# Performance work log

Measured on AMD Instinct MI355X. Metric: run time of the kernel, lower is better.

## Reference

```python
import jax, jax.numpy as jnp
import numpy as np

B, H, N, D = 4, 16, 2048, 128  # batch, num_head, maxlen, head_dim (qkdim == vdim)
EPS = 1e-6


def _act(x):
    # '1+elu' kernel feature map
    return jax.nn.elu(x) + 1.0


def _simple_rms_norm(x):
    # SimpleRMSNorm over the last dim: x / sqrt(mean(x^2) + eps), no learned scale
    ms = jnp.mean(jnp.square(x), axis=-1, keepdims=True)
    return x * jax.lax.rsqrt(ms + EPS)


def setup_inputs() -> dict:
    key = jax.random.key(0)
    kq, kk, kv, km = jax.random.split(key, 4)
    Q = jax.random.normal(kq, (B, H, N, D), dtype=jnp.float32)
    K = jax.random.normal(kk, (B, H, N, D), dtype=jnp.float32)
    V = jax.random.normal(kv, (B, H, N, D), dtype=jnp.float32)
    mask = jax.random.uniform(km, (B, N), dtype=jnp.float32)
    return {"Q": Q, "K": K, "V": V, "mask": mask}


def reference(Q, K, V, mask):
    m = mask[:, None, :, None]           # (B, 1, N, 1)
    Qf = _act(Q)                          # (B, H, N, D)
    Kf = _act(K) * m                      # masked feature-mapped keys
    Vf = V * m                            # masked values
    # non-causal linear attention: KV = sum_n K_n (x) V_n ; out = Q @ KV
    KV = jnp.einsum('bhnd,bhne->bhde', Kf, Vf)    # (B, H, D, D)
    out = jnp.einsum('bhde,bhnd->bhne', KV, Qf)   # (B, H, N, D)
    return _simple_rms_norm(out)
```

## Files before the change

### kernel.cpp

```cpp
#include <hip/hip_runtime.h>
#include <hip/hip_bf16.h>

#define NBH 64
#define NSEQ 2048
#define DD 128
#define EPS 1e-6f

typedef __bf16 bf16x8 __attribute__((ext_vector_type(8)));
typedef __bf16 bf16x4 __attribute__((ext_vector_type(4)));
typedef float  f32x4  __attribute__((ext_vector_type(4)));

__device__ __forceinline__ float elu1(float x) {
    return x > 0.f ? x + 1.f : __expf(x);
}

__device__ __forceinline__ int swz(int r) {
    return ((r >> 2) & 7) ^ ((r & 1) << 2);
}

__global__ __launch_bounds__(512, 4) void kv_partial_kernel(
    const float* __restrict__ K, const float* __restrict__ V,
    const float* __restrict__ mask, float* __restrict__ part)
{
    __shared__ __bf16 KfT[2][128 * 64];
    __shared__ __bf16 VfT[2][128 * 64];
    __shared__ float  mloc[256];

    const int s    = blockIdx.x;
    const int bh   = blockIdx.y;
    const int b    = bh >> 4;
    const int t    = threadIdx.x;
    const int lane = t & 63;
    const int w    = t >> 6;
    const int quad = lane >> 4;
    const int col  = lane & 15;
    const int n0   = s * 256;

    const int isV = t >> 8;
    const int c   = t & 31;
    const int rg  = (t >> 5) & 7;

    const f32x4* S4 = (const f32x4*)((isV ? V : K) + ((size_t)bh * NSEQ + n0) * DD);
    __bf16* myT = isV ? &VfT[0][0] : &KfT[0][0];

    f32x4 acc[8];
    #pragma unroll
    for (int nt = 0; nt < 8; ++nt) acc[nt] = (f32x4){0.f, 0.f, 0.f, 0.f};

    const int arow = w * 16 + col;
    const int aidx = arow * 64 + (swz(arow) << 3);
    int bidx[8];
    #pragma unroll
    for (int nt = 0; nt < 8; ++nt) {
        int r = nt * 16 + col;
        bidx[nt] = r * 64 + (swz(r) << 3);
    }

    f32x4 xr[8];

    auto load_tile = [&](int tile) {
        #pragma unroll
        for (int j = 0; j < 8; ++j)
            xr[j] = S4[(tile * 64 + rg * 8 + j) * 32 + c];
    };

    auto stage = [&](int buf, int tile) {
        float ml[8];
        #pragma unroll
        for (int j = 0; j < 8; ++j) ml[j] = mloc[tile * 64 + rg * 8 + j];
        __bf16* dst = myT + buf * (128 * 64);
        #pragma unroll
        for (int i = 0; i < 4; ++i) {
            bf16x8 xc;
            if (!isV) {
                #pragma unroll
                for (int j = 0; j < 8; ++j) xc[j] = (__bf16)(elu1(xr[j][i]) * ml[j]);
            } else {
                #pragma unroll
                for (int j = 0; j < 8; ++j) xc[j] = (__bf16)(xr[j][i] * ml[j]);
            }
            int d = 4 * c + i;
            *(bf16x8*)&dst[d * 64 + ((rg ^ swz(d)) << 3)] = xc;
        }
    };

    auto mfma_tile = [&](int buf) {
        const __bf16* Vb = &VfT[buf][0];
        const __bf16* Kb = &KfT[buf][0];
        #pragma unroll
        for (int kk = 0; kk < 2; ++kk) {
            int k0 = kk * 32 + quad * 8;
            bf16x8 a = *(bf16x8*)&Vb[aidx ^ k0];
            #pragma unroll
            for (int nt = 0; nt < 8; ++nt) {
                bf16x8 bb = *(bf16x8*)&Kb[bidx[nt] ^ k0];
                acc[nt] = __builtin_amdgcn_mfma_f32_16x16x32_bf16(a, bb, acc[nt], 0, 0, 0);
            }
        }
    };

    float mf = 0.f;
    if (t < 256) mf = mask[b * NSEQ + n0 + t];
    load_tile(0);
    if (t < 256) mloc[t] = mf;
    __syncthreads();
    stage(0, 0);
    __syncthreads();

    #pragma unroll
    for (int tile = 0; tile < 4; ++tile) {
        if (tile < 3) load_tile(tile + 1);
        mfma_tile(tile & 1);
        if (tile < 3) {
            stage((tile + 1) & 1, tile + 1);
            __syncthreads();
        }
    }

    float* po = part + (((size_t)bh * 8 + s) << 14);
    #pragma unroll
    for (int r = 0; r < 4; ++r) {
        int e = w * 16 + quad * 4 + r;
        #pragma unroll
        for (int nt = 0; nt < 8; ++nt)
            po[e * 128 + nt * 16 + col] = acc[nt][r];
    }
}

__global__ __launch_bounds__(256) void kv_reduce_kernel(
    const float* __restrict__ part, __bf16* __restrict__ kvt)
{
    int gid = blockIdx.x * 256 + threadIdx.x;
    int i   = gid * 4;
    int bh  = i >> 14;
    int ii  = i & 16383;
    const float* p = part + (((size_t)bh * 8) << 14) + ii;
    f32x4 sum = (f32x4){0.f, 0.f, 0.f, 0.f};
    #pragma unroll
    for (int s = 0; s < 8; ++s)
        sum += *(const f32x4*)(p + ((size_t)s << 14));
    bf16x4 o;
    o[0] = (__bf16)sum[0]; o[1] = (__bf16)sum[1];
    o[2] = (__bf16)sum[2]; o[3] = (__bf16)sum[3];
    *(bf16x4*)&kvt[i] = o;
}

__global__ __launch_bounds__(256, 4) void qkv_norm_kernel(
    const float* __restrict__ Q, const __bf16* __restrict__ kvt,
    float* __restrict__ out)
{
    __shared__ __bf16 KVT[128 * 136];

    const int bh   = blockIdx.y;
    const int row0 = blockIdx.x * 64;
    const int t    = threadIdx.x;
    const int lane = t & 63;
    const int w    = t >> 6;
    const int quad = lane >> 4;
    const int col  = lane & 15;

    const int row = row0 + w * 16 + col;
    const f32x4* q4 = (const f32x4*)(Q + ((size_t)bh * NSEQ + row) * DD);
    f32x4 qr[8];
    #pragma unroll
    for (int kk = 0; kk < 4; ++kk) {
        qr[2 * kk]     = q4[kk * 8 + quad * 2];
        qr[2 * kk + 1] = q4[kk * 8 + quad * 2 + 1];
    }

    {
        const __bf16* src = kvt + ((size_t)bh << 14);
        #pragma unroll
        for (int i = 0; i < 8; ++i) {
            int idx = i * 256 + t;
            int e   = idx >> 4;
            int dd  = (idx & 15) * 8;
            *(bf16x8*)&KVT[e * 136 + dd] = *(const bf16x8*)&src[e * 128 + dd];
        }
    }
    __syncthreads();

    bf16x8 a[4];
    #pragma unroll
    for (int kk = 0; kk < 4; ++kk) {
        #pragma unroll
        for (int h = 0; h < 2; ++h) {
            f32x4 q = qr[2 * kk + h];
            #pragma unroll
            for (int u = 0; u < 4; ++u)
                a[kk][h * 4 + u] = (__bf16)elu1(q[u]);
        }
    }

    f32x4 acc[8];
    #pragma unroll
    for (int et = 0; et < 8; ++et) acc[et] = (f32x4){0.f, 0.f, 0.f, 0.f};

    #pragma unroll
    for (int kk = 0; kk < 4; ++kk) {
        int k0 = kk * 32 + quad * 8;
        #pragma unroll
        for (int et = 0; et < 8; ++et) {
            bf16x8 bb = *(bf16x8*)&KVT[(et * 16 + col) * 136 + k0];
            acc[et] = __builtin_amdgcn_mfma_f32_16x16x32_bf16(a[kk], bb, acc[et], 0, 0, 0);
        }
    }

    float* ob = out + ((size_t)bh * NSEQ + row0) * DD;
    #pragma unroll
    for (int r = 0; r < 4; ++r) {
        float p = 0.f;
        #pragma unroll
        for (int et = 0; et < 8; ++et) p += acc[et][r] * acc[et][r];
        p += __shfl_xor(p, 1);
        p += __shfl_xor(p, 2);
        p += __shfl_xor(p, 4);
        p += __shfl_xor(p, 8);
        float scale = rsqrtf(p * (1.0f / 128.0f) + EPS);
        int orow = w * 16 + quad * 4 + r;
        #pragma unroll
        for (int et = 0; et < 8; ++et)
            ob[orow * DD + et * 16 + col] = acc[et][r] * scale;
    }
}

extern "C" void kernel_launch(void* const* d_in, const int* in_sizes, int n_in,
                              void* d_out, int out_size, void* d_ws, size_t ws_size,
                              hipStream_t stream) {
    const float* Q    = (const float*)d_in[0];
    const float* K    = (const float*)d_in[1];
    const float* V    = (const float*)d_in[2];
    const float* mask = (const float*)d_in[3];
    float* out = (float*)d_out;

    float*  part = (float*)d_ws;
    __bf16* kvt  = (__bf16*)((char*)d_ws + (size_t)NBH * 8 * 16384 * 4);

    kv_partial_kernel<<<dim3(8, NBH), 512, 0, stream>>>(K, V, mask, part);
    kv_reduce_kernel<<<1024, 256, 0, stream>>>(part, kvt);
    qkv_norm_kernel<<<dim3(32, NBH), 256, 0, stream>>>(Q, kvt, out);
}
```

Measured before the change: 236.6 us.

## Single-buffer KV partial LDS with 2D warp tiling; process two row chunks per Q block

The KV partial kernel drops double buffering in favor of a single LDS buffer guarded by extra barriers. Halving LDS use lets launch bounds ask for more resident blocks. Its warp tiling changes from 16-row strips to a 64x32 2D tile, so each warp loads fewer LDS fragments per MFMA. The Q/KV kernel now handles 128 rows per block in two chunks, reusing the staged KV^T tile and prefetching the second chunk's Q, at the cost of half as many blocks and more registers.

```diff
diff --git a/kernel.cpp b/kernel.cpp
--- a/kernel.cpp
+++ b/kernel.cpp
@@ -14,16 +14,17 @@
     return x > 0.f ? x + 1.f : __expf(x);
 }
 
-__device__ __forceinline__ int swz(int r) {
-    return ((r >> 2) & 7) ^ ((r & 1) << 2);
-}
-
-__global__ __launch_bounds__(512, 4) void kv_partial_kernel(
+__device__ __forceinline__ int ldsidx64(int r, int k0) {
+    int sw = ((((r >> 2) & 7) ^ ((r & 1) << 2)) << 3);
+    return r * 64 + (sw ^ k0);
+}
+
+__global__ __launch_bounds__(512, 6) void kv_partial_kernel(
     const float* __restrict__ K, const float* __restrict__ V,
     const float* __restrict__ mask, float* __restrict__ part)
 {
-    __shared__ __bf16 KfT[2][128 * 64];
-    __shared__ __bf16 VfT[2][128 * 64];
+    __shared__ __bf16 KfT[128 * 64];
+    __shared__ __bf16 VfT[128 * 64];
     __shared__ float  mloc[256];
 
     const int s    = blockIdx.x;
@@ -35,26 +36,19 @@
     const int quad = lane >> 4;
     const int col  = lane & 15;
     const int n0   = s * 256;
+    const int we   = w >> 2;
+    const int wd   = w & 3;
 
     const int isV = t >> 8;
     const int c   = t & 31;
     const int rg  = (t >> 5) & 7;
 
     const f32x4* S4 = (const f32x4*)((isV ? V : K) + ((size_t)bh * NSEQ + n0) * DD);
-    __bf16* myT = isV ? &VfT[0][0] : &KfT[0][0];
+    __bf16* myT = isV ? VfT : KfT;
 
     f32x4 acc[8];
     #pragma unroll
-    for (int nt = 0; nt < 8; ++nt) acc[nt] = (f32x4){0.f, 0.f, 0.f, 0.f};
-
-    const int arow = w * 16 + col;
-    const int aidx = arow * 64 + (swz(arow) << 3);
-    int bidx[8];
-    #pragma unroll
-    for (int nt = 0; nt < 8; ++nt) {
-        int r = nt * 16 + col;
-        bidx[nt] = r * 64 + (swz(r) << 3);
-    }
+    for (int i = 0; i < 8; ++i) acc[i] = (f32x4){0.f, 0.f, 0.f, 0.f};
 
     f32x4 xr[8];
 
@@ -64,11 +58,10 @@
             xr[j] = S4[(tile * 64 + rg * 8 + j) * 32 + c];
     };
 
-    auto stage = [&](int buf, int tile) {
+    auto stage = [&](int tile) {
         float ml[8];
         #pragma unroll
         for (int j = 0; j < 8; ++j) ml[j] = mloc[tile * 64 + rg * 8 + j];
-        __bf16* dst = myT + buf * (128 * 64);
         #pragma unroll
         for (int i = 0; i < 4; ++i) {
             bf16x8 xc;
@@ -80,50 +73,45 @@
                 for (int j = 0; j < 8; ++j) xc[j] = (__bf16)(xr[j][i] * ml[j]);
             }
             int d = 4 * c + i;
-            *(bf16x8*)&dst[d * 64 + ((rg ^ swz(d)) << 3)] = xc;
+            *(bf16x8*)&myT[ldsidx64(d, rg << 3)] = xc;
         }
     };
 
-    auto mfma_tile = [&](int buf) {
-        const __bf16* Vb = &VfT[buf][0];
-        const __bf16* Kb = &KfT[buf][0];
+    auto mfma_tile = [&]() {
         #pragma unroll
         for (int kk = 0; kk < 2; ++kk) {
             int k0 = kk * 32 + quad * 8;
-            bf16x8 a = *(bf16x8*)&Vb[aidx ^ k0];
-            #pragma unroll
-            for (int nt = 0; nt < 8; ++nt) {
-                bf16x8 bb = *(bf16x8*)&Kb[bidx[nt] ^ k0];
-                acc[nt] = __builtin_amdgcn_mfma_f32_16x16x32_bf16(a, bb, acc[nt], 0, 0, 0);
+            bf16x8 b0 = *(bf16x8*)&KfT[ldsidx64(wd * 32 + col, k0)];
+            bf16x8 b1 = *(bf16x8*)&KfT[ldsidx64(wd * 32 + 16 + col, k0)];
+            #pragma unroll
+            for (int at = 0; at < 4; ++at) {
+                bf16x8 aa = *(bf16x8*)&VfT[ldsidx64(we * 64 + at * 16 + col, k0)];
+                acc[at * 2]     = __builtin_amdgcn_mfma_f32_16x16x32_bf16(aa, b0, acc[at * 2], 0, 0, 0);
+                acc[at * 2 + 1] = __builtin_amdgcn_mfma_f32_16x16x32_bf16(aa, b1, acc[at * 2 + 1], 0, 0, 0);
             }
         }
     };
 
-    float mf = 0.f;
-    if (t < 256) mf = mask[b * NSEQ + n0 + t];
+    if (t < 256) mloc[t] = mask[b * NSEQ + n0 + t];
     load_tile(0);
-    if (t < 256) mloc[t] = mf;
     __syncthreads();
-    stage(0, 0);
+    stage(0);
     __syncthreads();
 
-    #pragma unroll
-    for (int tile = 0; tile < 4; ++tile) {
-        if (tile < 3) load_tile(tile + 1);
-        mfma_tile(tile & 1);
-        if (tile < 3) {
-            stage((tile + 1) & 1, tile + 1);
-            __syncthreads();
-        }
-    }
+    load_tile(1); mfma_tile(); __syncthreads(); stage(1); __syncthreads();
+    load_tile(2); mfma_tile(); __syncthreads(); stage(2); __syncthreads();
+    load_tile(3); mfma_tile(); __syncthreads(); stage(3); __syncthreads();
+    mfma_tile();
 
     float* po = part + (((size_t)bh * 8 + s) << 14);
     #pragma unroll
-    for (int r = 0; r < 4; ++r) {
-        int e = w * 16 + quad * 4 + r;
-        #pragma unroll
-        for (int nt = 0; nt < 8; ++nt)
-            po[e * 128 + nt * 16 + col] = acc[nt][r];
+    for (int at = 0; at < 4; ++at) {
+        #pragma unroll
+        for (int r = 0; r < 4; ++r) {
+            int e = we * 64 + at * 16 + quad * 4 + r;
+            po[e * 128 + wd * 32 + col]      = acc[at * 2][r];
+            po[e * 128 + wd * 32 + 16 + col] = acc[at * 2 + 1][r];
+        }
     }
 }
 
@@ -152,20 +140,21 @@
     __shared__ __bf16 KVT[128 * 136];
 
     const int bh   = blockIdx.y;
-    const int row0 = blockIdx.x * 64;
+    const int row0 = blockIdx.x * 128;
     const int t    = threadIdx.x;
     const int lane = t & 63;
     const int w    = t >> 6;
     const int quad = lane >> 4;
     const int col  = lane & 15;
 
-    const int row = row0 + w * 16 + col;
-    const f32x4* q4 = (const f32x4*)(Q + ((size_t)bh * NSEQ + row) * DD);
-    f32x4 qr[8];
+    const int qrow = w * 16 + col;
+    const f32x4* q4 = (const f32x4*)(Q + ((size_t)bh * NSEQ + row0 + qrow) * DD);
+
+    f32x4 qr0[8];
     #pragma unroll
     for (int kk = 0; kk < 4; ++kk) {
-        qr[2 * kk]     = q4[kk * 8 + quad * 2];
-        qr[2 * kk + 1] = q4[kk * 8 + quad * 2 + 1];
+        qr0[2 * kk]     = q4[kk * 8 + quad * 2];
+        qr0[2 * kk + 1] = q4[kk * 8 + quad * 2 + 1];
     }
 
     {
@@ -185,42 +174,66 @@
     for (int kk = 0; kk < 4; ++kk) {
         #pragma unroll
         for (int h = 0; h < 2; ++h) {
-            f32x4 q = qr[2 * kk + h];
+            f32x4 q = qr0[2 * kk + h];
             #pragma unroll
             for (int u = 0; u < 4; ++u)
                 a[kk][h * 4 + u] = (__bf16)elu1(q[u]);
         }
     }
 
-    f32x4 acc[8];
-    #pragma unroll
-    for (int et = 0; et < 8; ++et) acc[et] = (f32x4){0.f, 0.f, 0.f, 0.f};
-
+    f32x4 qr1[8];
     #pragma unroll
     for (int kk = 0; kk < 4; ++kk) {
-        int k0 = kk * 32 + quad * 8;
-        #pragma unroll
-        for (int et = 0; et < 8; ++et) {
-            bf16x8 bb = *(bf16x8*)&KVT[(et * 16 + col) * 136 + k0];
-            acc[et] = __builtin_amdgcn_mfma_f32_16x16x32_bf16(a[kk], bb, acc[et], 0, 0, 0);
-        }
+        qr1[2 * kk]     = q4[2048 + kk * 8 + quad * 2];
+        qr1[2 * kk + 1] = q4[2048 + kk * 8 + quad * 2 + 1];
     }
 
     float* ob = out + ((size_t)bh * NSEQ + row0) * DD;
-    #pragma unroll
-    for (int r = 0; r < 4; ++r) {
-        float p = 0.f;
-        #pragma unroll
-        for (int et = 0; et < 8; ++et) p += acc[et][r] * acc[et][r];
-        p += __shfl_xor(p, 1);
-        p += __shfl_xor(p, 2);
-        p += __shfl_xor(p, 4);
-        p += __shfl_xor(p, 8);
-        float scale = rsqrtf(p * (1.0f / 128.0f) + EPS);
-        int orow = w * 16 + quad * 4 + r;
-        #pragma unroll
-        for (int et = 0; et < 8; ++et)
-            ob[orow * DD + et * 16 + col] = acc[et][r] * scale;
+
+    #pragma unroll
+    for (int chunk = 0; chunk < 2; ++chunk) {
+        f32x4 acc[8];
+        #pragma unroll
+        for (int et = 0; et < 8; ++et) acc[et] = (f32x4){0.f, 0.f, 0.f, 0.f};
+
+        #pragma unroll
+        for (int kk = 0; kk < 4; ++kk) {
+            int k0 = kk * 32 + quad * 8;
+            #pragma unroll
+            for (int et = 0; et < 8; ++et) {
+                bf16x8 bb = *(bf16x8*)&KVT[(et * 16 + col) * 136 + k0];
+                acc[et] = __builtin_amdgcn_mfma_f32_16x16x32_bf16(a[kk], bb, acc[et], 0, 0, 0);
+            }
+        }
+
+        #pragma unroll
+        for (int r = 0; r < 4; ++r) {
+            float p = 0.f;
+            #pragma unroll
+            for (int et = 0; et < 8; ++et) p += acc[et][r] * acc[et][r];
+            p += __shfl_xor(p, 1);
+            p += __shfl_xor(p, 2);
+            p += __shfl_xor(p, 4);
+            p += __shfl_xor(p, 8);
+            float scale = rsqrtf(p * (1.0f / 128.0f) + EPS);
+            int orow = chunk * 64 + w * 16 + quad * 4 + r;
+            #pragma unroll
+            for (int et = 0; et < 8; ++et)
+                ob[orow * DD + et * 16 + col] = acc[et][r] * scale;
+        }
+
+        if (chunk == 0) {
+            #pragma unroll
+            for (int kk = 0; kk < 4; ++kk) {
+                #pragma unroll
+                for (int h = 0; h < 2; ++h) {
+                    f32x4 q = qr1[2 * kk + h];
+                    #pragma unroll
+                    for (int u = 0; u < 4; ++u)
+                        a[kk][h * 4 + u] = (__bf16)elu1(q[u]);
+                }
+            }
+        }
     }
 }
 
@@ -238,5 +251,5 @@
 
     kv_partial_kernel<<<dim3(8, NBH), 512, 0, stream>>>(K, V, mask, part);
     kv_reduce_kernel<<<1024, 256, 0, stream>>>(part, kvt);
-    qkv_norm_kernel<<<dim3(32, NBH), 256, 0, stream>>>(Q, kvt, out);
-}
+    qkv_norm_kernel<<<dim3(16, NBH), 256, 0, stream>>>(Q, kvt, out);
+}
```

Measured after the change: 251.5 us. 6.3% more time.

## Fuse three kernels into one cooperative kernel with grid-wide syncs

Applied to the files above, without the earlier changes.

Replaces the partial-KV, reduce, and Q·KV+RMSNorm launches with a single cooperative kernel of 512 blocks that uses grid.sync() between the phases. Each block then handles 256 query rows in two chunks, and shared memory is unioned across the phases. This removes two kernel launch gaps and the tail idle time between them. In exchange it pays for two grid-wide barriers and lower parallelism in the final phase (512 blocks instead of 2048), and it falls back to the three-kernel path if the cooperative launch fails.

```diff
diff --git a/kernel.cpp b/kernel.cpp
--- a/kernel.cpp
+++ b/kernel.cpp
@@ -1,5 +1,8 @@
 #include <hip/hip_runtime.h>
 #include <hip/hip_bf16.h>
+#include <hip/hip_cooperative_groups.h>
+
+namespace cg = cooperative_groups;
 
 #define NBH 64
 #define NSEQ 2048
@@ -18,13 +21,24 @@
     return ((r >> 2) & 7) ^ ((r & 1) << 2);
 }
 
-__global__ __launch_bounds__(512, 4) void kv_partial_kernel(
-    const float* __restrict__ K, const float* __restrict__ V,
-    const float* __restrict__ mask, float* __restrict__ part)
+struct SmemA {
+    __bf16 KfT[2][128 * 64];
+    __bf16 VfT[2][128 * 64];
+    float  mloc[256];
+};
+
+__global__ __launch_bounds__(512, 4) void fused_kernel(
+    const float* __restrict__ Q, const float* __restrict__ K,
+    const float* __restrict__ V, const float* __restrict__ mask,
+    float* __restrict__ part, __bf16* __restrict__ kvt,
+    float* __restrict__ out)
 {
-    __shared__ __bf16 KfT[2][128 * 64];
-    __shared__ __bf16 VfT[2][128 * 64];
-    __shared__ float  mloc[256];
+    __shared__ union __align__(16) {
+        SmemA  a;
+        __bf16 kvtile[128 * 136];
+    } sm;
+
+    cg::grid_group grid = cg::this_grid();
 
     const int s    = blockIdx.x;
     const int bh   = blockIdx.y;
@@ -36,6 +50,223 @@
     const int col  = lane & 15;
     const int n0   = s * 256;
 
+    {
+        const int isV = t >> 8;
+        const int c   = t & 31;
+        const int rg  = (t >> 5) & 7;
+
+        const f32x4* S4 = (const f32x4*)((isV ? V : K) + ((size_t)bh * NSEQ + n0) * DD);
+        __bf16* myT = isV ? &sm.a.VfT[0][0] : &sm.a.KfT[0][0];
+
+        f32x4 acc[8];
+        #pragma unroll
+        for (int nt = 0; nt < 8; ++nt) acc[nt] = (f32x4){0.f, 0.f, 0.f, 0.f};
+
+        const int arow = w * 16 + col;
+        const int aidx = arow * 64 + (swz(arow) << 3);
+        int bidx[8];
+        #pragma unroll
+        for (int nt = 0; nt < 8; ++nt) {
+            int r = nt * 16 + col;
+            bidx[nt] = r * 64 + (swz(r) << 3);
+        }
+
+        f32x4 xr[8];
+
+        auto load_tile = [&](int tile) {
+            #pragma unroll
+            for (int j = 0; j < 8; ++j)
+                xr[j] = S4[(tile * 64 + rg * 8 + j) * 32 + c];
+        };
+
+        auto stage = [&](int buf, int tile) {
+            float ml[8];
+            #pragma unroll
+            for (int j = 0; j < 8; ++j) ml[j] = sm.a.mloc[tile * 64 + rg * 8 + j];
+            __bf16* dst = myT + buf * (128 * 64);
+            #pragma unroll
+            for (int i = 0; i < 4; ++i) {
+                bf16x8 xc;
+                if (!isV) {
+                    #pragma unroll
+                    for (int j = 0; j < 8; ++j) xc[j] = (__bf16)(elu1(xr[j][i]) * ml[j]);
+                } else {
+                    #pragma unroll
+                    for (int j = 0; j < 8; ++j) xc[j] = (__bf16)(xr[j][i] * ml[j]);
+                }
+                int d = 4 * c + i;
+                *(bf16x8*)&dst[d * 64 + ((rg ^ swz(d)) << 3)] = xc;
+            }
+        };
+
+        auto mfma_tile = [&](int buf) {
+            const __bf16* Vb = &sm.a.VfT[buf][0];
+            const __bf16* Kb = &sm.a.KfT[buf][0];
+            #pragma unroll
+            for (int kk = 0; kk < 2; ++kk) {
+                int k0 = kk * 32 + quad * 8;
+                bf16x8 a = *(bf16x8*)&Vb[aidx ^ k0];
+                #pragma unroll
+                for (int nt = 0; nt < 8; ++nt) {
+                    bf16x8 bb = *(bf16x8*)&Kb[bidx[nt] ^ k0];
+                    acc[nt] = __builtin_amdgcn_mfma_f32_16x16x32_bf16(a, bb, acc[nt], 0, 0, 0);
+                }
+            }
+        };
+
+        if (t < 256) sm.a.mloc[t] = mask[b * NSEQ + n0 + t];
+        load_tile(0);
+        __syncthreads();
+        stage(0, 0);
+        __syncthreads();
+
+        #pragma unroll
+        for (int tile = 0; tile < 4; ++tile) {
+            if (tile < 3) load_tile(tile + 1);
+            mfma_tile(tile & 1);
+            if (tile < 3) {
+                stage((tile + 1) & 1, tile + 1);
+                __syncthreads();
+            }
+        }
+
+        float* po = part + (((size_t)bh * 8 + s) << 14);
+        #pragma unroll
+        for (int r = 0; r < 4; ++r) {
+            int e = w * 16 + quad * 4 + r;
+            #pragma unroll
+            for (int nt = 0; nt < 8; ++nt)
+                po[e * 128 + nt * 16 + col] = acc[nt][r];
+        }
+    }
+
+    grid.sync();
+
+    {
+        int ii = s * 2048 + t * 4;
+        const float* p = part + (((size_t)bh * 8) << 14) + ii;
+        f32x4 sum = (f32x4){0.f, 0.f, 0.f, 0.f};
+        #pragma unroll
+        for (int ps = 0; ps < 8; ++ps)
+            sum += *(const f32x4*)(p + ((size_t)ps << 14));
+        bf16x4 o;
+        o[0] = (__bf16)sum[0]; o[1] = (__bf16)sum[1];
+        o[2] = (__bf16)sum[2]; o[3] = (__bf16)sum[3];
+        *(bf16x4*)&kvt[((size_t)bh << 14) + ii] = o;
+    }
+
+    grid.sync();
+
+    {
+        const int qrow = w * 16 + col;
+        const f32x4* q4 = (const f32x4*)(Q + ((size_t)bh * NSEQ + n0 + qrow) * DD);
+
+        f32x4 qr0[8];
+        #pragma unroll
+        for (int kk = 0; kk < 4; ++kk) {
+            qr0[2 * kk]     = q4[kk * 8 + quad * 2];
+            qr0[2 * kk + 1] = q4[kk * 8 + quad * 2 + 1];
+        }
+
+        {
+            const __bf16* src = kvt + ((size_t)bh << 14);
+            #pragma unroll
+            for (int i = 0; i < 4; ++i) {
+                int idx = i * 512 + t;
+                int e   = idx >> 4;
+                int dd  = (idx & 15) * 8;
+                *(bf16x8*)&sm.kvtile[e * 136 + dd] = *(const bf16x8*)&src[e * 128 + dd];
+            }
+        }
+        __syncthreads();
+
+        bf16x8 afr[4];
+        #pragma unroll
+        for (int kk = 0; kk < 4; ++kk) {
+            #pragma unroll
+            for (int h = 0; h < 2; ++h) {
+                f32x4 q = qr0[2 * kk + h];
+                #pragma unroll
+                for (int u = 0; u < 4; ++u)
+                    afr[kk][h * 4 + u] = (__bf16)elu1(q[u]);
+            }
+        }
+
+        f32x4 qr1[8];
+        #pragma unroll
+        for (int kk = 0; kk < 4; ++kk) {
+            qr1[2 * kk]     = q4[4096 + kk * 8 + quad * 2];
+            qr1[2 * kk + 1] = q4[4096 + kk * 8 + quad * 2 + 1];
+        }
+
+        float* ob = out + ((size_t)bh * NSEQ + n0) * DD;
+
+        #pragma unroll
+        for (int chunk = 0; chunk < 2; ++chunk) {
+            f32x4 acc[8];
+            #pragma unroll
+            for (int et = 0; et < 8; ++et) acc[et] = (f32x4){0.f, 0.f, 0.f, 0.f};
+
+            #pragma unroll
+            for (int kk = 0; kk < 4; ++kk) {
+                int k0 = kk * 32 + quad * 8;
+                #pragma unroll
+                for (int et = 0; et < 8; ++et) {
+                    bf16x8 bb = *(bf16x8*)&sm.kvtile[(et * 16 + col) * 136 + k0];
+                    acc[et] = __builtin_amdgcn_mfma_f32_16x16x32_bf16(afr[kk], bb, acc[et], 0, 0, 0);
+                }
+            }
+
+            #pragma unroll
+            for (int r = 0; r < 4; ++r) {
+                float p = 0.f;
+                #pragma unroll
+                for (int et = 0; et < 8; ++et) p += acc[et][r] * acc[et][r];
+                p += __shfl_xor(p, 1);
+                p += __shfl_xor(p, 2);
+                p += __shfl_xor(p, 4);
+                p += __shfl_xor(p, 8);
+                float scale = rsqrtf(p * (1.0f / 128.0f) + EPS);
+                int orow = chunk * 128 + w * 16 + quad * 4 + r;
+                #pragma unroll
+                for (int et = 0; et < 8; ++et)
+                    ob[orow * DD + et * 16 + col] = acc[et][r] * scale;
+            }
+
+            if (chunk == 0) {
+                #pragma unroll
+                for (int kk = 0; kk < 4; ++kk) {
+                    #pragma unroll
+                    for (int h = 0; h < 2; ++h) {
+                        f32x4 q = qr1[2 * kk + h];
+                        #pragma unroll
+                        for (int u = 0; u < 4; ++u)
+                            afr[kk][h * 4 + u] = (__bf16)elu1(q[u]);
+                    }
+                }
+            }
+        }
+    }
+}
+
+__global__ __launch_bounds__(512, 4) void kv_partial_kernel(
+    const float* __restrict__ K, const float* __restrict__ V,
+    const float* __restrict__ mask, float* __restrict__ part)
+{
+    __shared__ __bf16 KfT[2][128 * 64];
+    __shared__ __bf16 VfT[2][128 * 64];
+    __shared__ float  mloc[256];
+
+    const int s    = blockIdx.x;
+    const int bh   = blockIdx.y;
+    const int b    = bh >> 4;
+    const int t    = threadIdx.x;
+    const int lane = t & 63;
+    const int w    = t >> 6;
+    const int quad = lane >> 4;
+    const int col  = lane & 15;
+    const int n0   = s * 256;
+
     const int isV = t >> 8;
     const int c   = t & 31;
     const int rg  = (t >> 5) & 7;
@@ -63,7 +294,6 @@
         for (int j = 0; j < 8; ++j)
             xr[j] = S4[(tile * 64 + rg * 8 + j) * 32 + c];
     };
-
     auto stage = [&](int buf, int tile) {
         float ml[8];
         #pragma unroll
@@ -83,7 +313,6 @@
             *(bf16x8*)&dst[d * 64 + ((rg ^ swz(d)) << 3)] = xc;
         }
     };
-
     auto mfma_tile = [&](int buf) {
         const __bf16* Vb = &VfT[buf][0];
         const __bf16* Kb = &KfT[buf][0];
@@ -99,10 +328,8 @@
         }
     };
 
-    float mf = 0.f;
-    if (t < 256) mf = mask[b * NSEQ + n0 + t];
+    if (t < 256) mloc[t] = mask[b * NSEQ + n0 + t];
     load_tile(0);
-    if (t < 256) mloc[t] = mf;
     __syncthreads();
     stage(0, 0);
     __syncthreads();
@@ -236,7 +463,14 @@
     float*  part = (float*)d_ws;
     __bf16* kvt  = (__bf16*)((char*)d_ws + (size_t)NBH * 8 * 16384 * 4);
 
-    kv_partial_kernel<<<dim3(8, NBH), 512, 0, stream>>>(K, V, mask, part);
-    kv_reduce_kernel<<<1024, 256, 0, stream>>>(part, kvt);
-    qkv_norm_kernel<<<dim3(32, NBH), 256, 0, stream>>>(Q, kvt, out);
-}
+    void* args[] = {(void*)&Q, (void*)&K, (void*)&V, (void*)&mask,
+                    (void*)&part, (void*)&kvt, (void*)&out};
+    hipError_t e = hipLaunchCooperativeKernel((const void*)fused_kernel,
+                                              dim3(8, NBH), dim3(512),
+                                              args, 0, stream);
+    if (e != hipSuccess) {
+        kv_partial_kernel<<<dim3(8, NBH), 512, 0, stream>>>(K, V, mask, part);
+        kv_reduce_kernel<<<1024, 256, 0, stream>>>(part, kvt);
+        qkv_norm_kernel<<<dim3(32, NBH), 256, 0, stream>>>(Q, kvt, out);
+    }
+}
```

Result: slower. 373.5 us (+57.9%).
